# Performance work log

Hardware: AMD Instinct MI355X
Metric: run time of the kernel (lower is better)

## Reference

```python
import jax, jax.numpy as jnp
import numpy as np

B, Hs, Ws, DIM = 1, 48, 48, 768
NUM_HEADS, HEAD_DIM = 12, 64
RANK, ALPHA = 4, 1.0
SCALING = ALPHA / RANK
SCALE = HEAD_DIM ** -0.5


def setup_inputs() -> dict:
    key = jax.random.key(0)
    ks = jax.random.split(key, 13)
    s = lambda k, shape, sc=0.02: jax.random.normal(k, shape, jnp.float32) * sc
    return dict(
        x=jax.random.normal(ks[0], (B, Hs, Ws, DIM), jnp.float32),
        qkv_w=s(ks[1], (3 * DIM, DIM)),
        qkv_b=s(ks[2], (3 * DIM,)),
        proj_w=s(ks[3], (DIM, DIM)),
        proj_b=s(ks[4], (DIM,)),
        rel_pos_h=s(ks[5], (2 * Hs - 1, HEAD_DIM)),
        rel_pos_w=s(ks[6], (2 * Ws - 1, HEAD_DIM)),
        lora_q_A=s(ks[7], (RANK, DIM)),
        lora_q_B=s(ks[8], (DIM, RANK)),
        lora_k_A=s(ks[9], (RANK, DIM)),
        lora_k_B=s(ks[10], (DIM, RANK)),
        lora_v_A=s(ks[11], (RANK, DIM)),
        lora_v_B=s(ks[12], (DIM, RANK)),
    )


def _get_rel_pos(size, rel_pos):
    # q_size == k_size -> relative index = i - j + (size - 1)
    coords = jnp.arange(size)
    idx = coords[:, None] - coords[None, :] + (size - 1)
    return rel_pos[idx]  # [size, size, head_dim]


def reference(x, qkv_w, qkv_b, proj_w, proj_b, rel_pos_h, rel_pos_w,
              lora_q_A, lora_q_B, lora_k_A, lora_k_B, lora_v_A, lora_v_B):
    Bn, Hq, Wq, dim = x.shape
    N = Hq * Wq
    x_flat = x.reshape(Bn, N, dim)
    # frozen base qkv: [B, N, 3, nh, hd] -> [3, B, nh, N, hd]
    qkv = (x_flat @ qkv_w.T + qkv_b).reshape(Bn, N, 3, NUM_HEADS, HEAD_DIM)
    qkv = jnp.transpose(qkv, (2, 0, 3, 1, 4))

    def lora(A, Bm):
        d = (x_flat @ A.T @ Bm.T) * SCALING  # [B, N, dim]
        return jnp.transpose(d.reshape(Bn, N, NUM_HEADS, HEAD_DIM), (0, 2, 1, 3))

    q = (qkv[0] + lora(lora_q_A, lora_q_B)).reshape(Bn * NUM_HEADS, N, HEAD_DIM)
    k = (qkv[1] + lora(lora_k_A, lora_k_B)).reshape(Bn * NUM_HEADS, N, HEAD_DIM)
    v = (qkv[2] + lora(lora_v_A, lora_v_B)).reshape(Bn * NUM_HEADS, N, HEAD_DIM)

    attn = (q * SCALE) @ jnp.swapaxes(k, -2, -1)  # [B*nh, N, N]

    # decomposed relative position bias
    Rh = _get_rel_pos(Hq, rel_pos_h)  # [H, H, hd]
    Rw = _get_rel_pos(Wq, rel_pos_w)  # [W, W, hd]
    r_q = q.reshape(Bn * NUM_HEADS, Hq, Wq, HEAD_DIM)
    rel_h = jnp.einsum("bhwc,hkc->bhwk", r_q, Rh)
    rel_w = jnp.einsum("bhwc,wkc->bhwk", r_q, Rw)
    attn = (attn.reshape(-1, Hq, Wq, Hq, Wq)
            + rel_h[:, :, :, :, None]
            + rel_w[:, :, :, None, :]).reshape(-1, N, N)

    attn = jax.nn.softmax(attn, axis=-1)
    out = (attn @ v).reshape(Bn, NUM_HEADS, Hq, Wq, HEAD_DIM)
    out = jnp.transpose(out, (0, 2, 3, 1, 4)).reshape(Bn, Hq, Wq, dim)
    return out @ proj_w.T + proj_b
```

## Files before the change

kernel.cpp:

```cpp
#include <hip/hip_runtime.h>

#define NTOK 2304
#define NH 12
#define HD 64

typedef __attribute__((ext_vector_type(8))) short bf16x8;
typedef __attribute__((ext_vector_type(4))) float f32x4;

__device__ __forceinline__ unsigned short f2bf(float f){
  union { float f; unsigned u; } v; v.f = f;
  unsigned r = v.u + 0x7fffu + ((v.u >> 16) & 1u);
  return (unsigned short)(r >> 16);
}
__device__ __forceinline__ float bf2f(unsigned short h){
  union { unsigned u; float f; } v; v.u = ((unsigned)h) << 16;
  return v.f;
}
__device__ __forceinline__ void gload_lds16(const void* g, void* lds){
  __builtin_amdgcn_global_load_lds(
    (const __attribute__((address_space(1))) unsigned int*)g,
    (__attribute__((address_space(3))) unsigned int*)lds, 16, 0, 0);
}

__global__ __launch_bounds__(256) void cvt_all(
    const float* __restrict__ x, const float* __restrict__ qw, const float* __restrict__ pw,
    unsigned short* __restrict__ xb, unsigned short* __restrict__ wqb, unsigned short* __restrict__ wpb){
  int i = blockIdx.x * 256 + threadIdx.x;
  const float* src; unsigned short* dst; int off;
  if (i < 442368)      { src = x;  dst = xb;  off = i; }
  else if (i < 884736) { src = qw; dst = wqb; off = i - 442368; }
  else                 { src = pw; dst = wpb; off = i - 884736; }
  float4 v = ((const float4*)src)[off];
  union { unsigned short u[4]; unsigned long long ll; } o;
  o.u[0] = f2bf(v.x); o.u[1] = f2bf(v.y); o.u[2] = f2bf(v.z); o.u[3] = f2bf(v.w);
  ((unsigned long long*)dst)[off] = o.ll;
}

__global__ __launch_bounds__(256) void lora_t_kernel(const float* __restrict__ x,
    const float* __restrict__ Aq, const float* __restrict__ Ak, const float* __restrict__ Av,
    float* __restrict__ t){
  int wave = (blockIdx.x * 256 + threadIdx.x) >> 6;
  int lane = threadIdx.x & 63;
  if (wave >= NTOK) return;
  const float* xr = x + (size_t)wave * 768;
  float part[12];
  #pragma unroll
  for (int j = 0; j < 12; j++) part[j] = 0.f;
  for (int k = lane; k < 768; k += 64){
    float xv = xr[k];
    #pragma unroll
    for (int r = 0; r < 4; r++){
      part[r]     += xv * Aq[r*768 + k];
      part[4 + r] += xv * Ak[r*768 + k];
      part[8 + r] += xv * Av[r*768 + k];
    }
  }
  #pragma unroll
  for (int j = 0; j < 12; j++){
    float v = part[j];
    #pragma unroll
    for (int off = 32; off; off >>= 1) v += __shfl_xor(v, off);
    if (lane == 0){
      int mat = j >> 2, r = j & 3;
      t[((size_t)mat * NTOK + wave) * 4 + r] = v;
    }
  }
}

__global__ __launch_bounds__(256) void qkv_gemm(
    const unsigned short* __restrict__ xg,
    const unsigned short* __restrict__ wg,
    const float* __restrict__ bias,
    const float* __restrict__ t,
    const float* __restrict__ Bq, const float* __restrict__ Bk, const float* __restrict__ Bv,
    unsigned short* __restrict__ qo,
    unsigned short* __restrict__ ko,
    unsigned short* __restrict__ vT)
{
  __shared__ short As[128*64];
  __shared__ short Bs[64*64];
  const int tid = threadIdx.x;
  const int lane = tid & 63;
  const int wv = tid >> 6;
  const int r = lane & 15, g = lane >> 4;
  const int wm = (wv >> 1) * 64, wn = (wv & 1) * 32;
  const int m0 = blockIdx.y * 128, n0 = blockIdx.x * 64;

  f32x4 acc[4][2];
  #pragma unroll
  for (int i = 0; i < 4; i++)
    #pragma unroll
    for (int j = 0; j < 2; j++) acc[i][j] = (f32x4){0.f, 0.f, 0.f, 0.f};

  for (int k0 = 0; k0 < 768; k0 += 64){
    __syncthreads();
    #pragma unroll
    for (int it = 0; it < 4; it++){
      int f = it * 256 + tid;
      int row = f >> 3, u = f & 7;
      int us = ((u ^ (row & 7)) << 3);
      gload_lds16(xg + (size_t)(m0 + row) * 768 + k0 + us, &As[f * 8]);
    }
    #pragma unroll
    for (int it = 0; it < 2; it++){
      int f = it * 256 + tid;
      int row = f >> 3, u = f & 7;
      int us = ((u ^ (row & 7)) << 3);
      gload_lds16(wg + (size_t)(n0 + row) * 768 + k0 + us, &Bs[f * 8]);
    }
    __syncthreads();
    #pragma unroll
    for (int ks = 0; ks < 2; ks++){
      bf16x8 af[4], bfr[2];
      #pragma unroll
      for (int mt = 0; mt < 4; mt++){
        int row = wm + mt * 16 + r;
        af[mt] = *(const bf16x8*)&As[row * 64 + ((((ks << 2) | g) ^ (r & 7)) << 3)];
      }
      #pragma unroll
      for (int nt = 0; nt < 2; nt++){
        int row = wn + nt * 16 + r;
        bfr[nt] = *(const bf16x8*)&Bs[row * 64 + ((((ks << 2) | g) ^ (r & 7)) << 3)];
      }
      #pragma unroll
      for (int mt = 0; mt < 4; mt++)
        #pragma unroll
        for (int nt = 0; nt < 2; nt++)
          acc[mt][nt] = __builtin_amdgcn_mfma_f32_16x16x32_bf16(af[mt], bfr[nt], acc[mt][nt], 0, 0, 0);
    }
  }

  const int part = n0 / 768;
  const float* Bl = (part == 0) ? Bq : ((part == 1) ? Bk : Bv);
  const float* tp = t + (size_t)part * NTOK * 4;
  #pragma unroll
  for (int mt = 0; mt < 4; mt++){
    #pragma unroll
    for (int reg = 0; reg < 4; reg++){
      int row_m = m0 + wm + mt * 16 + g * 4 + reg;
      float4 tv = *(const float4*)&tp[row_m * 4];
      #pragma unroll
      for (int nt = 0; nt < 2; nt++){
        int col = n0 + wn + nt * 16 + r;
        int cc = col - part * 768;
        float4 bw = *(const float4*)&Bl[cc * 4];
        float val = acc[mt][nt][reg] + bias[col]
                  + 0.25f * (tv.x * bw.x + tv.y * bw.y + tv.z * bw.z + tv.w * bw.w);
        int head = cc >> 6, d = cc & 63;
        if (part == 0)      qo[((size_t)head * NTOK + row_m) * 64 + d] = f2bf(val * 0.125f);
        else if (part == 1) ko[((size_t)head * NTOK + row_m) * 64 + d] = f2bf(val);
        else                vT[((size_t)head * 64 + d) * NTOK + row_m] = f2bf(val);
      }
    }
  }
}

__global__ __launch_bounds__(256, 2) void rel_gemm(
    const unsigned short* __restrict__ qg,
    const float* __restrict__ rph,
    const float* __restrict__ rpw,
    float* __restrict__ rel_h,
    float* __restrict__ rel_w)
{
  __shared__ float G[48 * 196];
  const int ih = blockIdx.x, head = blockIdx.y;
  const int tid = threadIdx.x, lane = tid & 63, wv = tid >> 6;
  const int r = lane & 15, g = lane >> 4;
  const int q0 = ih * 48;

  bf16x8 af[3][2];
  #pragma unroll
  for (int mt = 0; mt < 3; mt++)
    #pragma unroll
    for (int ks = 0; ks < 2; ks++)
      af[mt][ks] = *(const bf16x8*)&qg[((size_t)head * NTOK + q0 + mt * 16 + r) * 64 + ks * 32 + g * 8];

  bf16x8 bfv[3][2];
  #pragma unroll
  for (int nt = 0; nt < 3; nt++){
    int col = wv * 48 + nt * 16 + r;
    const float* src = (col < 95) ? &rph[(size_t)col * 64]
                     : (col < 190) ? &rpw[(size_t)(col - 95) * 64]
                     : &rpw[0];
    #pragma unroll
    for (int ks = 0; ks < 2; ks++){
      float4 lo = *(const float4*)&src[ks * 32 + g * 8];
      float4 hi = *(const float4*)&src[ks * 32 + g * 8 + 4];
      union { unsigned short u[8]; bf16x8 v; } t;
      t.u[0] = f2bf(lo.x); t.u[1] = f2bf(lo.y); t.u[2] = f2bf(lo.z); t.u[3] = f2bf(lo.w);
      t.u[4] = f2bf(hi.x); t.u[5] = f2bf(hi.y); t.u[6] = f2bf(hi.z); t.u[7] = f2bf(hi.w);
      bfv[nt][ks] = t.v;
    }
  }

  f32x4 acc[3][3];
  #pragma unroll
  for (int mt = 0; mt < 3; mt++)
    #pragma unroll
    for (int nt = 0; nt < 3; nt++) acc[mt][nt] = (f32x4){0.f, 0.f, 0.f, 0.f};
  #pragma unroll
  for (int ks = 0; ks < 2; ks++)
    #pragma unroll
    for (int mt = 0; mt < 3; mt++)
      #pragma unroll
      for (int nt = 0; nt < 3; nt++)
        acc[mt][nt] = __builtin_amdgcn_mfma_f32_16x16x32_bf16(af[mt][ks], bfv[nt][ks], acc[mt][nt], 0, 0, 0);

  #pragma unroll
  for (int mt = 0; mt < 3; mt++)
    #pragma unroll
    for (int reg = 0; reg < 4; reg++){
      int row = mt * 16 + g * 4 + reg;
      #pragma unroll
      for (int nt = 0; nt < 3; nt++)
        G[row * 196 + wv * 48 + nt * 16 + r] = acc[mt][nt][reg];
    }
  __syncthreads();

  for (int idx = tid; idx < 48 * 96; idx += 256){
    int i = idx / 96, c = idx % 96;
    size_t gi = (size_t)head * NTOK + q0 + i;
    if (c < 48) rel_h[gi * 48 + c]        = G[i * 196 + (ih + 47 - c)] * 8.f;
    else        rel_w[gi * 48 + (c - 48)] = G[i * 196 + 95 + (i + 47 - (c - 48))] * 8.f;
  }
}

__global__ __launch_bounds__(256, 3) void attn_kernel(
    const unsigned short* __restrict__ qg,
    const unsigned short* __restrict__ kg,
    const unsigned short* __restrict__ vT,
    const float* __restrict__ rel_h,
    const float* __restrict__ rel_w,
    unsigned short* __restrict__ ao)
{
  __shared__ __align__(16) char smem[46336];
  unsigned short* Ks = (unsigned short*)smem;
  unsigned short* Vs = (unsigned short*)(smem + 16384);
  float* relH = (float*)(smem + 32768);
  float* lsh = (float*)(smem + 46080);

  const int head = blockIdx.y;
  const int q0 = blockIdx.x * 64;
  const int tid = threadIdx.x, lane = tid & 63, wv = tid >> 6;
  const int r = lane & 15, g = lane >> 4;

  const unsigned short* kbase = kg + (size_t)head * NTOK * 64;
  const unsigned short* vbase = vT + (size_t)head * 64 * NTOK;

  for (int idx = tid; idx < 64 * 12; idx += 256){
    int i = idx / 12, c4 = idx % 12;
    *(float4*)&relH[i * 52 + c4 * 4] =
        *(const float4*)&rel_h[((size_t)head * NTOK + q0 + i) * 48 + c4 * 4];
  }

  float4 wreg[3];
  #pragma unroll
  for (int j = 0; j < 3; j++)
    wreg[j] = *(const float4*)&rel_w[((size_t)head * NTOK + q0 + wv * 16 + r) * 48 + j * 16 + g * 4];

  bf16x8 qf[2];
  #pragma unroll
  for (int ks = 0; ks < 2; ks++)
    qf[ks] = *(const bf16x8*)&qg[((size_t)head * NTOK + q0 + wv * 16 + r) * 64 + ks * 32 + g * 8];

  const int rowIn = lane >> 3, uu = lane & 7;

  #pragma unroll
  for (int s2 = 0; s2 < 2; s2++){
    int seg = wv * 2 + s2;
    int row = seg * 8 + rowIn;
    gload_lds16(kbase + (size_t)row * 64 + ((uu ^ (row & 7)) << 3), &Ks[seg * 512 + lane * 8]);
    gload_lds16(vbase + (size_t)row * NTOK + ((uu ^ (row & 7)) << 3), &Vs[seg * 512 + lane * 8]);
  }
  __syncthreads();

  f32x4 Oa[4];
  float lrun = 0.f;
  #pragma unroll
  for (int dt = 0; dt < 4; dt++) Oa[dt] = (f32x4){0.f, 0.f, 0.f, 0.f};

  const float* rsh = &relH[(wv * 16 + r) * 52];

  const int KH_T[3][4] = {{0,0,0,1},{1,1,2,2},{2,3,3,3}};
  const int J_T[3][4]  = {{0,1,2,0},{1,2,0,1},{2,0,1,2}};

  const int srcA = r + ((g & 1) << 5);
  const int srcB = srcA + 16;
  const int hi = (g >> 1);

  int buf = 0;
  for (int a = 0; a < 12; a++){
    #pragma unroll
    for (int tb = 0; tb < 3; tb++){
      const int t = a * 3 + tb;
      unsigned short* KsB = &Ks[buf * 4096];
      unsigned short* VsB = &Vs[buf * 4096];

      if (t < 35){
        const int key0n = (t + 1) * 64;
        unsigned short* KsN = &Ks[(buf ^ 1) * 4096];
        unsigned short* VsN = &Vs[(buf ^ 1) * 4096];
        #pragma unroll
        for (int s2 = 0; s2 < 2; s2++){
          int seg = wv * 2 + s2;
          int row = seg * 8 + rowIn;
          gload_lds16(kbase + (size_t)(key0n + row) * 64 + ((uu ^ (row & 7)) << 3),
                      &KsN[seg * 512 + lane * 8]);
          gload_lds16(vbase + (size_t)row * NTOK + key0n + ((uu ^ (row & 7)) << 3),
                      &VsN[seg * 512 + lane * 8]);
        }
      }

      f32x4 s[4];
      __builtin_amdgcn_s_setprio(1);
      #pragma unroll
      for (int ntl = 0; ntl < 4; ntl++){
        bf16x8 kc0 = *(const bf16x8*)&KsB[(ntl * 16 + r) * 64 + ((g ^ (r & 7)) << 3)];
        bf16x8 kc1 = *(const bf16x8*)&KsB[(ntl * 16 + r) * 64 + (((4 + g) ^ (r & 7)) << 3)];
        s[ntl] = (f32x4){0.f, 0.f, 0.f, 0.f};
        s[ntl] = __builtin_amdgcn_mfma_f32_16x16x32_bf16(kc0, qf[0], s[ntl], 0, 0, 0);
        s[ntl] = __builtin_amdgcn_mfma_f32_16x16x32_bf16(kc1, qf[1], s[ntl], 0, 0, 0);
      }
      __builtin_amdgcn_s_setprio(0);

      unsigned W0[4], W1[4];
      #pragma unroll
      for (int ntl = 0; ntl < 4; ntl++){
        float bh = rsh[4 * a + KH_T[tb][ntl]];
        float4 w = wreg[J_T[tb][ntl]];
        float p0 = __expf(s[ntl][0] + bh + w.x);
        float p1 = __expf(s[ntl][1] + bh + w.y);
        float p2 = __expf(s[ntl][2] + bh + w.z);
        float p3 = __expf(s[ntl][3] + bh + w.w);
        lrun += (p0 + p1) + (p2 + p3);
        asm("v_cvt_pk_bf16_f32 %0, %1, %2" : "=v"(W0[ntl]) : "v"(p0), "v"(p1));
        asm("v_cvt_pk_bf16_f32 %0, %1, %2" : "=v"(W1[ntl]) : "v"(p2), "v"(p3));
      }

      bf16x8 pf[2];
      #pragma unroll
      for (int ks = 0; ks < 2; ks++){
        unsigned a0 = (unsigned)__shfl((int)W0[2*ks],   srcA);
        unsigned a1 = (unsigned)__shfl((int)W0[2*ks+1], srcA);
        unsigned b0 = (unsigned)__shfl((int)W1[2*ks],   srcA);
        unsigned b1 = (unsigned)__shfl((int)W1[2*ks+1], srcA);
        unsigned c0 = (unsigned)__shfl((int)W0[2*ks],   srcB);
        unsigned c1 = (unsigned)__shfl((int)W0[2*ks+1], srcB);
        unsigned d0 = (unsigned)__shfl((int)W1[2*ks],   srcB);
        unsigned d1 = (unsigned)__shfl((int)W1[2*ks+1], srcB);
        union { unsigned w[4]; bf16x8 v; } u;
        u.w[0] = hi ? a1 : a0;
        u.w[1] = hi ? b1 : b0;
        u.w[2] = hi ? c1 : c0;
        u.w[3] = hi ? d1 : d0;
        pf[ks] = u.v;
      }

      __builtin_amdgcn_s_setprio(1);
      #pragma unroll
      for (int dt = 0; dt < 4; dt++){
        #pragma unroll
        for (int ks = 0; ks < 2; ks++){
          bf16x8 vf = *(const bf16x8*)&VsB[(dt * 16 + r) * 64 + (((ks * 4 + g) ^ (r & 7)) << 3)];
          Oa[dt] = __builtin_amdgcn_mfma_f32_16x16x32_bf16(pf[ks], vf, Oa[dt], 0, 0, 0);
        }
      }
      __builtin_amdgcn_s_setprio(0);

      __syncthreads();
      buf ^= 1;
    }
  }

  {
    float l = lrun;
    l += __shfl_xor(l, 16);
    l += __shfl_xor(l, 32);
    if (lane < 16) lsh[wv * 16 + lane] = l;
  }
  __syncthreads();
  float invL[4];
  #pragma unroll
  for (int reg = 0; reg < 4; reg++) invL[reg] = 1.f / lsh[wv * 16 + g * 4 + reg];
  #pragma unroll
  for (int dt = 0; dt < 4; dt++)
    #pragma unroll
    for (int reg = 0; reg < 4; reg++){
      int token = q0 + wv * 16 + g * 4 + reg;
      ao[(size_t)token * 768 + head * 64 + dt * 16 + r] = f2bf(Oa[dt][reg] * invL[reg]);
    }
}

__global__ __launch_bounds__(256) void proj_gemm(
    const unsigned short* __restrict__ ag,
    const unsigned short* __restrict__ wg,
    const float* __restrict__ bias,
    float* __restrict__ out)
{
  __shared__ short As[64*64];
  __shared__ short Bs[64*64];
  const int tid = threadIdx.x;
  const int lane = tid & 63;
  const int wv = tid >> 6;
  const int r = lane & 15, g = lane >> 4;
  const int wm = (wv >> 1) * 32, wn = (wv & 1) * 32;
  const int m0 = blockIdx.y * 64, n0 = blockIdx.x * 64;

  f32x4 acc[2][2];
  #pragma unroll
  for (int i = 0; i < 2; i++)
    #pragma unroll
    for (int j = 0; j < 2; j++) acc[i][j] = (f32x4){0.f, 0.f, 0.f, 0.f};

  for (int k0 = 0; k0 < 768; k0 += 64){
    __syncthreads();
    #pragma unroll
    for (int it = 0; it < 2; it++){
      int f = it * 256 + tid;
      int row = f >> 3, u = f & 7;
      int us = ((u ^ (row & 7)) << 3);
      gload_lds16(ag + (size_t)(m0 + row) * 768 + k0 + us, &As[f * 8]);
      gload_lds16(wg + (size_t)(n0 + row) * 768 + k0 + us, &Bs[f * 8]);
    }
    __syncthreads();
    #pragma unroll
    for (int ks = 0; ks < 2; ks++){
      bf16x8 af[2], bfr[2];
      #pragma unroll
      for (int mt = 0; mt < 2; mt++){
        int row = wm + mt * 16 + r;
        af[mt] = *(const bf16x8*)&As[row * 64 + ((((ks << 2) | g) ^ (r & 7)) << 3)];
      }
      #pragma unroll
      for (int nt = 0; nt < 2; nt++){
        int row = wn + nt * 16 + r;
        bfr[nt] = *(const bf16x8*)&Bs[row * 64 + ((((ks << 2) | g) ^ (r & 7)) << 3)];
      }
      #pragma unroll
      for (int mt = 0; mt < 2; mt++)
        #pragma unroll
        for (int nt = 0; nt < 2; nt++)
          acc[mt][nt] = __builtin_amdgcn_mfma_f32_16x16x32_bf16(af[mt], bfr[nt], acc[mt][nt], 0, 0, 0);
    }
  }

  #pragma unroll
  for (int mt = 0; mt < 2; mt++)
    #pragma unroll
    for (int reg = 0; reg < 4; reg++){
      int row_m = m0 + wm + mt * 16 + g * 4 + reg;
      #pragma unroll
      for (int nt = 0; nt < 2; nt++){
        int col = n0 + wn + nt * 16 + r;
        out[(size_t)row_m * 768 + col] = acc[mt][nt][reg] + bias[col];
      }
    }
}

extern "C" void kernel_launch(void* const* d_in, const int* in_sizes, int n_in,
                              void* d_out, int out_size, void* d_ws, size_t ws_size,
                              hipStream_t stream){
  (void)in_sizes; (void)n_in; (void)out_size; (void)ws_size;
  const float* x      = (const float*)d_in[0];
  const float* qkv_w  = (const float*)d_in[1];
  const float* qkv_b  = (const float*)d_in[2];
  const float* proj_w = (const float*)d_in[3];
  const float* proj_b = (const float*)d_in[4];
  const float* rph    = (const float*)d_in[5];
  const float* rpw    = (const float*)d_in[6];
  const float* Aq     = (const float*)d_in[7];
  const float* Bq     = (const float*)d_in[8];
  const float* Ak     = (const float*)d_in[9];
  const float* Bk     = (const float*)d_in[10];
  const float* Av     = (const float*)d_in[11];
  const float* Bv     = (const float*)d_in[12];

  char* w = (char*)d_ws;
  unsigned short* xb  = (unsigned short*)(w + 0);
  unsigned short* wqb = (unsigned short*)(w + 3538944);
  unsigned short* wpb = (unsigned short*)(w + 7077888);
  unsigned short* qb  = (unsigned short*)(w + 8257536);
  unsigned short* kb  = (unsigned short*)(w + 11796480);
  unsigned short* vtb = (unsigned short*)(w + 15335424);
  float* tb           = (float*)(w + 18874368);
  float* rhb          = (float*)(w + 18984960);
  float* rwb          = (float*)(w + 24293376);
  unsigned short* aob = (unsigned short*)(w + 29601792);

  cvt_all<<<4032, 256, 0, stream>>>(x, qkv_w, proj_w, xb, wqb, wpb);
  lora_t_kernel<<<576, 256, 0, stream>>>(x, Aq, Ak, Av, tb);
  qkv_gemm<<<dim3(36, 18), 256, 0, stream>>>(xb, wqb, qkv_b, tb, Bq, Bk, Bv, qb, kb, vtb);
  rel_gemm<<<dim3(48, 12), 256, 0, stream>>>(qb, rph, rpw, rhb, rwb);
  attn_kernel<<<dim3(36, 12), 256, 0, stream>>>(qb, kb, vtb, rhb, rwb, aob);
  proj_gemm<<<dim3(12, 36), 256, 0, stream>>>(aob, wpb, proj_b, (float*)d_out);
}
```

Measured before the change: 110.9 us.

## Triple-buffer K/V tiles in attention with prefetch distance two

Replaces the double-buffered K/V LDS staging with a three-slot ring that prefetches two tiles ahead, using explicit vmcnt waits so each barrier only waits for the tile about to be consumed. The aim is to hide global-to-LDS load latency better than one-ahead prefetching. In exchange, LDS per block grows to about 62 KB and launch bounds drop from 3 to 2 blocks per CU, which lowers occupancy.

```diff
diff --git a/kernel.cpp b/kernel.cpp
--- a/kernel.cpp
+++ b/kernel.cpp
@@ -225,7 +225,7 @@
   }
 }
 
-__global__ __launch_bounds__(256, 3) void attn_kernel(
+__global__ __launch_bounds__(256, 2) void attn_kernel(
     const unsigned short* __restrict__ qg,
     const unsigned short* __restrict__ kg,
     const unsigned short* __restrict__ vT,
@@ -233,11 +233,11 @@
     const float* __restrict__ rel_w,
     unsigned short* __restrict__ ao)
 {
-  __shared__ __align__(16) char smem[46336];
+  __shared__ __align__(16) char smem[62720];
   unsigned short* Ks = (unsigned short*)smem;
-  unsigned short* Vs = (unsigned short*)(smem + 16384);
-  float* relH = (float*)(smem + 32768);
-  float* lsh = (float*)(smem + 46080);
+  unsigned short* Vs = (unsigned short*)(smem + 24576);
+  float* relH = (float*)(smem + 49152);
+  float* lsh = (float*)(smem + 62464);
 
   const int head = blockIdx.y;
   const int q0 = blockIdx.x * 64;
@@ -265,13 +265,21 @@
 
   const int rowIn = lane >> 3, uu = lane & 7;
 
-  #pragma unroll
-  for (int s2 = 0; s2 < 2; s2++){
-    int seg = wv * 2 + s2;
-    int row = seg * 8 + rowIn;
-    gload_lds16(kbase + (size_t)row * 64 + ((uu ^ (row & 7)) << 3), &Ks[seg * 512 + lane * 8]);
-    gload_lds16(vbase + (size_t)row * NTOK + ((uu ^ (row & 7)) << 3), &Vs[seg * 512 + lane * 8]);
-  }
+#define STAGE_TILE(T, SLOT) do { \
+    const int key0_ = (T) * 64; \
+    _Pragma("unroll") \
+    for (int s2 = 0; s2 < 2; s2++){ \
+      int seg = wv * 2 + s2; \
+      int row = seg * 8 + rowIn; \
+      gload_lds16(kbase + (size_t)(key0_ + row) * 64 + ((uu ^ (row & 7)) << 3), \
+                  &Ks[(SLOT) * 4096 + seg * 512 + lane * 8]); \
+      gload_lds16(vbase + (size_t)row * NTOK + key0_ + ((uu ^ (row & 7)) << 3), \
+                  &Vs[(SLOT) * 4096 + seg * 512 + lane * 8]); \
+    } \
+  } while(0)
+
+  STAGE_TILE(0, 0);
+  STAGE_TILE(1, 1);
   __syncthreads();
 
   f32x4 Oa[4];
@@ -288,28 +296,16 @@
   const int srcB = srcA + 16;
   const int hi = (g >> 1);
 
-  int buf = 0;
   for (int a = 0; a < 12; a++){
     #pragma unroll
     for (int tb = 0; tb < 3; tb++){
       const int t = a * 3 + tb;
-      unsigned short* KsB = &Ks[buf * 4096];
-      unsigned short* VsB = &Vs[buf * 4096];
-
-      if (t < 35){
-        const int key0n = (t + 1) * 64;
-        unsigned short* KsN = &Ks[(buf ^ 1) * 4096];
-        unsigned short* VsN = &Vs[(buf ^ 1) * 4096];
-        #pragma unroll
-        for (int s2 = 0; s2 < 2; s2++){
-          int seg = wv * 2 + s2;
-          int row = seg * 8 + rowIn;
-          gload_lds16(kbase + (size_t)(key0n + row) * 64 + ((uu ^ (row & 7)) << 3),
-                      &KsN[seg * 512 + lane * 8]);
-          gload_lds16(vbase + (size_t)row * NTOK + key0n + ((uu ^ (row & 7)) << 3),
-                      &VsN[seg * 512 + lane * 8]);
-        }
-      }
+      const int slot  = tb;
+      const int slot2 = (tb + 2) % 3;
+      unsigned short* KsB = &Ks[slot * 4096];
+      unsigned short* VsB = &Vs[slot * 4096];
+
+      if (t < 34) STAGE_TILE(t + 2, slot2);
 
       f32x4 s[4];
       __builtin_amdgcn_s_setprio(1);
@@ -367,10 +363,12 @@
       }
       __builtin_amdgcn_s_setprio(0);
 
-      __syncthreads();
-      buf ^= 1;
-    }
-  }
+      if (t < 34)      asm volatile("s_waitcnt vmcnt(4)" ::: "memory");
+      else             asm volatile("s_waitcnt vmcnt(0)" ::: "memory");
+      __builtin_amdgcn_s_barrier();
+    }
+  }
+#undef STAGE_TILE
 
   {
     float l = lrun;
```

New measurement: 111.7 us. Within noise of the previous version (+0.7%).

## Process two query subtiles per wave in attention, halving block threads

Applied to the files above, without the earlier changes.

The attention kernel now runs 2 waves per block instead of 4, and each wave handles 32 query rows as two 16-row subtiles. Each K and V fragment read from LDS is reused for two MFMAs, which halves LDS reads per unit of work. Each wave now issues twice as many async global-to-LDS loads per tile. The cost is higher register pressure from the doubled accumulators and score tiles, fewer waves per block for latency hiding, and a lower launch-bounds occupancy hint.

```diff
diff --git a/kernel.cpp b/kernel.cpp
--- a/kernel.cpp
+++ b/kernel.cpp
@@ -225,7 +225,7 @@
   }
 }
 
-__global__ __launch_bounds__(256, 3) void attn_kernel(
+__global__ __launch_bounds__(128, 2) void attn_kernel(
     const unsigned short* __restrict__ qg,
     const unsigned short* __restrict__ kg,
     const unsigned short* __restrict__ vT,
@@ -247,39 +247,46 @@
   const unsigned short* kbase = kg + (size_t)head * NTOK * 64;
   const unsigned short* vbase = vT + (size_t)head * 64 * NTOK;
 
-  for (int idx = tid; idx < 64 * 12; idx += 256){
+  for (int idx = tid; idx < 64 * 12; idx += 128){
     int i = idx / 12, c4 = idx % 12;
     *(float4*)&relH[i * 52 + c4 * 4] =
         *(const float4*)&rel_h[((size_t)head * NTOK + q0 + i) * 48 + c4 * 4];
   }
 
-  float4 wreg[3];
-  #pragma unroll
-  for (int j = 0; j < 3; j++)
-    wreg[j] = *(const float4*)&rel_w[((size_t)head * NTOK + q0 + wv * 16 + r) * 48 + j * 16 + g * 4];
-
-  bf16x8 qf[2];
-  #pragma unroll
-  for (int ks = 0; ks < 2; ks++)
-    qf[ks] = *(const bf16x8*)&qg[((size_t)head * NTOK + q0 + wv * 16 + r) * 64 + ks * 32 + g * 8];
+  float4 wreg[2][3];
+  #pragma unroll
+  for (int qm = 0; qm < 2; qm++)
+    #pragma unroll
+    for (int j = 0; j < 3; j++)
+      wreg[qm][j] = *(const float4*)&rel_w[((size_t)head * NTOK + q0 + wv * 32 + qm * 16 + r) * 48 + j * 16 + g * 4];
+
+  bf16x8 qf[2][2];
+  #pragma unroll
+  for (int qm = 0; qm < 2; qm++)
+    #pragma unroll
+    for (int ks = 0; ks < 2; ks++)
+      qf[qm][ks] = *(const bf16x8*)&qg[((size_t)head * NTOK + q0 + wv * 32 + qm * 16 + r) * 64 + ks * 32 + g * 8];
 
   const int rowIn = lane >> 3, uu = lane & 7;
 
   #pragma unroll
-  for (int s2 = 0; s2 < 2; s2++){
-    int seg = wv * 2 + s2;
+  for (int s4 = 0; s4 < 4; s4++){
+    int seg = wv * 4 + s4;
     int row = seg * 8 + rowIn;
     gload_lds16(kbase + (size_t)row * 64 + ((uu ^ (row & 7)) << 3), &Ks[seg * 512 + lane * 8]);
     gload_lds16(vbase + (size_t)row * NTOK + ((uu ^ (row & 7)) << 3), &Vs[seg * 512 + lane * 8]);
   }
   __syncthreads();
 
-  f32x4 Oa[4];
-  float lrun = 0.f;
-  #pragma unroll
-  for (int dt = 0; dt < 4; dt++) Oa[dt] = (f32x4){0.f, 0.f, 0.f, 0.f};
-
-  const float* rsh = &relH[(wv * 16 + r) * 52];
+  f32x4 Oa[2][4];
+  float lrun[2] = {0.f, 0.f};
+  #pragma unroll
+  for (int qm = 0; qm < 2; qm++)
+    #pragma unroll
+    for (int dt = 0; dt < 4; dt++) Oa[qm][dt] = (f32x4){0.f, 0.f, 0.f, 0.f};
+
+  const float* rsh0 = &relH[(wv * 32 + r) * 52];
+  const float* rsh1 = &relH[(wv * 32 + 16 + r) * 52];
 
   const int KH_T[3][4] = {{0,0,0,1},{1,1,2,2},{2,3,3,3}};
   const int J_T[3][4]  = {{0,1,2,0},{1,2,0,1},{2,0,1,2}};
@@ -301,8 +308,8 @@
         unsigned short* KsN = &Ks[(buf ^ 1) * 4096];
         unsigned short* VsN = &Vs[(buf ^ 1) * 4096];
         #pragma unroll
-        for (int s2 = 0; s2 < 2; s2++){
-          int seg = wv * 2 + s2;
+        for (int s4 = 0; s4 < 4; s4++){
+          int seg = wv * 4 + s4;
           int row = seg * 8 + rowIn;
           gload_lds16(kbase + (size_t)(key0n + row) * 64 + ((uu ^ (row & 7)) << 3),
                       &KsN[seg * 512 + lane * 8]);
@@ -311,50 +318,60 @@
         }
       }
 
-      f32x4 s[4];
+      f32x4 s[4][2];
       __builtin_amdgcn_s_setprio(1);
       #pragma unroll
       for (int ntl = 0; ntl < 4; ntl++){
         bf16x8 kc0 = *(const bf16x8*)&KsB[(ntl * 16 + r) * 64 + ((g ^ (r & 7)) << 3)];
         bf16x8 kc1 = *(const bf16x8*)&KsB[(ntl * 16 + r) * 64 + (((4 + g) ^ (r & 7)) << 3)];
-        s[ntl] = (f32x4){0.f, 0.f, 0.f, 0.f};
-        s[ntl] = __builtin_amdgcn_mfma_f32_16x16x32_bf16(kc0, qf[0], s[ntl], 0, 0, 0);
-        s[ntl] = __builtin_amdgcn_mfma_f32_16x16x32_bf16(kc1, qf[1], s[ntl], 0, 0, 0);
+        #pragma unroll
+        for (int qm = 0; qm < 2; qm++){
+          s[ntl][qm] = (f32x4){0.f, 0.f, 0.f, 0.f};
+          s[ntl][qm] = __builtin_amdgcn_mfma_f32_16x16x32_bf16(kc0, qf[qm][0], s[ntl][qm], 0, 0, 0);
+          s[ntl][qm] = __builtin_amdgcn_mfma_f32_16x16x32_bf16(kc1, qf[qm][1], s[ntl][qm], 0, 0, 0);
+        }
       }
       __builtin_amdgcn_s_setprio(0);
 
-      unsigned W0[4], W1[4];
+      unsigned W0[4][2], W1[4][2];
       #pragma unroll
       for (int ntl = 0; ntl < 4; ntl++){
-        float bh = rsh[4 * a + KH_T[tb][ntl]];
-        float4 w = wreg[J_T[tb][ntl]];
-        float p0 = __expf(s[ntl][0] + bh + w.x);
-        float p1 = __expf(s[ntl][1] + bh + w.y);
-        float p2 = __expf(s[ntl][2] + bh + w.z);
-        float p3 = __expf(s[ntl][3] + bh + w.w);
-        lrun += (p0 + p1) + (p2 + p3);
-        asm("v_cvt_pk_bf16_f32 %0, %1, %2" : "=v"(W0[ntl]) : "v"(p0), "v"(p1));
-        asm("v_cvt_pk_bf16_f32 %0, %1, %2" : "=v"(W1[ntl]) : "v"(p2), "v"(p3));
-      }
-
-      bf16x8 pf[2];
-      #pragma unroll
-      for (int ks = 0; ks < 2; ks++){
-        unsigned a0 = (unsigned)__shfl((int)W0[2*ks],   srcA);
-        unsigned a1 = (unsigned)__shfl((int)W0[2*ks+1], srcA);
-        unsigned b0 = (unsigned)__shfl((int)W1[2*ks],   srcA);
-        unsigned b1 = (unsigned)__shfl((int)W1[2*ks+1], srcA);
-        unsigned c0 = (unsigned)__shfl((int)W0[2*ks],   srcB);
-        unsigned c1 = (unsigned)__shfl((int)W0[2*ks+1], srcB);
-        unsigned d0 = (unsigned)__shfl((int)W1[2*ks],   srcB);
-        unsigned d1 = (unsigned)__shfl((int)W1[2*ks+1], srcB);
-        union { unsigned w[4]; bf16x8 v; } u;
-        u.w[0] = hi ? a1 : a0;
-        u.w[1] = hi ? b1 : b0;
-        u.w[2] = hi ? c1 : c0;
-        u.w[3] = hi ? d1 : d0;
-        pf[ks] = u.v;
-      }
+        const int kh = 4 * a + KH_T[tb][ntl];
+        const int j  = J_T[tb][ntl];
+        float bh[2] = { rsh0[kh], rsh1[kh] };
+        #pragma unroll
+        for (int qm = 0; qm < 2; qm++){
+          float4 w = wreg[qm][j];
+          float p0 = __expf(s[ntl][qm][0] + bh[qm] + w.x);
+          float p1 = __expf(s[ntl][qm][1] + bh[qm] + w.y);
+          float p2 = __expf(s[ntl][qm][2] + bh[qm] + w.z);
+          float p3 = __expf(s[ntl][qm][3] + bh[qm] + w.w);
+          lrun[qm] += (p0 + p1) + (p2 + p3);
+          asm("v_cvt_pk_bf16_f32 %0, %1, %2" : "=v"(W0[ntl][qm]) : "v"(p0), "v"(p1));
+          asm("v_cvt_pk_bf16_f32 %0, %1, %2" : "=v"(W1[ntl][qm]) : "v"(p2), "v"(p3));
+        }
+      }
+
+      bf16x8 pf[2][2];
+      #pragma unroll
+      for (int qm = 0; qm < 2; qm++)
+        #pragma unroll
+        for (int ks = 0; ks < 2; ks++){
+          unsigned a0 = (unsigned)__shfl((int)W0[2*ks][qm],   srcA);
+          unsigned a1 = (unsigned)__shfl((int)W0[2*ks+1][qm], srcA);
+          unsigned b0 = (unsigned)__shfl((int)W1[2*ks][qm],   srcA);
+          unsigned b1 = (unsigned)__shfl((int)W1[2*ks+1][qm], srcA);
+          unsigned c0 = (unsigned)__shfl((int)W0[2*ks][qm],   srcB);
+          unsigned c1 = (unsigned)__shfl((int)W0[2*ks+1][qm], srcB);
+          unsigned d0 = (unsigned)__shfl((int)W1[2*ks][qm],   srcB);
+          unsigned d1 = (unsigned)__shfl((int)W1[2*ks+1][qm], srcB);
+          union { unsigned w[4]; bf16x8 v; } u;
+          u.w[0] = hi ? a1 : a0;
+          u.w[1] = hi ? b1 : b0;
+          u.w[2] = hi ? c1 : c0;
+          u.w[3] = hi ? d1 : d0;
+          pf[qm][ks] = u.v;
+        }
 
       __builtin_amdgcn_s_setprio(1);
       #pragma unroll
@@ -362,7 +379,9 @@
         #pragma unroll
         for (int ks = 0; ks < 2; ks++){
           bf16x8 vf = *(const bf16x8*)&VsB[(dt * 16 + r) * 64 + (((ks * 4 + g) ^ (r & 7)) << 3)];
-          Oa[dt] = __builtin_amdgcn_mfma_f32_16x16x32_bf16(pf[ks], vf, Oa[dt], 0, 0, 0);
+          #pragma unroll
+          for (int qm = 0; qm < 2; qm++)
+            Oa[qm][dt] = __builtin_amdgcn_mfma_f32_16x16x32_bf16(pf[qm][ks], vf, Oa[qm][dt], 0, 0, 0);
         }
       }
       __builtin_amdgcn_s_setprio(0);
@@ -372,23 +391,27 @@
     }
   }
 
-  {
-    float l = lrun;
+  #pragma unroll
+  for (int qm = 0; qm < 2; qm++){
+    float l = lrun[qm];
     l += __shfl_xor(l, 16);
     l += __shfl_xor(l, 32);
-    if (lane < 16) lsh[wv * 16 + lane] = l;
+    if (lane < 16) lsh[wv * 32 + qm * 16 + lane] = l;
   }
   __syncthreads();
-  float invL[4];
-  #pragma unroll
-  for (int reg = 0; reg < 4; reg++) invL[reg] = 1.f / lsh[wv * 16 + g * 4 + reg];
-  #pragma unroll
-  for (int dt = 0; dt < 4; dt++)
-    #pragma unroll
-    for (int reg = 0; reg < 4; reg++){
-      int token = q0 + wv * 16 + g * 4 + reg;
-      ao[(size_t)token * 768 + head * 64 + dt * 16 + r] = f2bf(Oa[dt][reg] * invL[reg]);
-    }
+  #pragma unroll
+  for (int qm = 0; qm < 2; qm++){
+    float invL[4];
+    #pragma unroll
+    for (int reg = 0; reg < 4; reg++) invL[reg] = 1.f / lsh[wv * 32 + qm * 16 + g * 4 + reg];
+    #pragma unroll
+    for (int dt = 0; dt < 4; dt++)
+      #pragma unroll
+      for (int reg = 0; reg < 4; reg++){
+        int token = q0 + wv * 32 + qm * 16 + g * 4 + reg;
+        ao[(size_t)token * 768 + head * 64 + dt * 16 + r] = f2bf(Oa[qm][dt][reg] * invL[reg]);
+      }
+  }
 }
 
 __global__ __launch_bounds__(256) void proj_gemm(
@@ -491,6 +514,6 @@
   lora_t_kernel<<<576, 256, 0, stream>>>(x, Aq, Ak, Av, tb);
   qkv_gemm<<<dim3(36, 18), 256, 0, stream>>>(xb, wqb, qkv_b, tb, Bq, Bk, Bv, qb, kb, vtb);
   rel_gemm<<<dim3(48, 12), 256, 0, stream>>>(qb, rph, rpw, rhb, rwb);
-  attn_kernel<<<dim3(36, 12), 256, 0, stream>>>(qb, kb, vtb, rhb, rwb, aob);
+  attn_kernel<<<dim3(36, 12), 128, 0, stream>>>(qb, kb, vtb, rhb, rwb, aob);
   proj_gemm<<<dim3(12, 36), 256, 0, stream>>>(aob, wpb, proj_b, (float*)d_out);
 }
```

Measured after the change: 130.9 us. 18.0% more time.
